# Kernel tuning notes

Hardware: AMD Instinct MI355X
Metric: run time of the kernel (lower is better)

## Reference

```python
import jax, jax.numpy as jnp
import numpy as np

HEADS = 6
EPS = 1e-5


def _na_idx(L, k, d):
    # NATTEN-style dilated neighborhood: work within dilation cosets,
    # clamp window to stay inside the image (window shifts at borders).
    i = np.arange(L)
    g = i % d
    p = i // d
    Lg = (L - g + d - 1) // d  # coset length per position
    start = np.clip(p - k // 2, 0, Lg - k)
    j = np.arange(k)
    nbr = g[:, None] + d * (start[:, None] + j[None, :])          # [L,k] neighbor coords
    rel = (start[:, None] + j[None, :]) - p[:, None] + (k - 1)    # [L,k] rpb index in [0,2k-2]
    return jnp.asarray(nbr, jnp.int32), jnp.asarray(rel, jnp.int32)


def _na2d(x, qkv_w, qkv_b, proj_w, proj_b, rpb, heads, k, d):
    # x: [B,H,W,C] NHWC neighborhood attention with relative positional bias
    B, H, W, C = x.shape
    dh = C // heads
    scale = dh ** -0.5
    qkv = (x @ qkv_w + qkv_b).reshape(B, H, W, 3, heads, dh)
    qkv = jnp.transpose(qkv, (3, 0, 4, 1, 2, 5))  # [3,B,h,H,W,dh]
    q, kk, v = qkv[0] * scale, qkv[1], qkv[2]
    nh, rh = _na_idx(H, k, d)
    nw, rw = _na_idx(W, k, d)

    def gather(t):  # [B,h,H,W,dh] -> [B,h,H,W,k,k,dh]
        t = t[:, :, nh]              # [B,h,H,k,W,dh]
        t = t[:, :, :, :, nw]        # [B,h,H,k,W,k,dh]
        return jnp.transpose(t, (0, 1, 2, 4, 3, 5, 6))

    kn, vn = gather(kk), gather(v)
    attn = jnp.einsum('bhxyd,bhxyijd->bhxyij', q, kn)  # [B,h,H,W,k,k]
    bias = rpb[:, rh]                  # [h,H,k,2k-1]
    bias = bias[:, :, :, rw]           # [h,H,k,W,k]
    bias = jnp.transpose(bias, (0, 1, 3, 2, 4))  # [h,H,W,k,k]
    attn = attn + bias[None]
    attn = jax.nn.softmax(attn.reshape(B, heads, H, W, k * k), axis=-1)
    attn = attn.reshape(B, heads, H, W, k, k)
    out = jnp.einsum('bhxyij,bhxyijd->bhxyd', attn, vn)
    out = jnp.transpose(out, (0, 2, 3, 1, 4)).reshape(B, H, W, C)
    return out @ proj_w + proj_b


def _rln(x, w, b, m1_w, m1_b, m2_w, m2_b):
    # Revised LayerNorm: normalize over (C,H,W) per sample; meta1/meta2 are 1x1 convs on std/mean
    mean = jnp.mean(x, axis=(1, 2, 3), keepdims=True)
    std = jnp.sqrt(jnp.mean((x - mean) ** 2, axis=(1, 2, 3), keepdims=True) + EPS)
    out = (x - mean) / std * w + b
    rescale = m1_w[None, :, None, None] * std + m1_b[None, :, None, None]
    rebias = m2_w[None, :, None, None] * mean + m2_b[None, :, None, None]
    return out, rescale, rebias


def _c11(x, w, b):  # 1x1 conv on NCHW == per-pixel linear
    return jnp.einsum('bchw,oc->bohw', x, w) + b[None, :, None, None]


def _gelu(x):
    return jax.nn.gelu(x, approximate=False)


def reference(x, ln_w, ln_b, m1_w, m1_b, m2_w, m2_b, qkv1_w, qkv1_b, proj1_w, proj1_b, rpb1, qkv2_w, qkv2_b, proj2_w, proj2_b, rpb2, mlp_w1, mlp_b1, mlp_w2, mlp_b2, bn_g, bn_b, bn_m, bn_v, pa_w1, pa_b1, pa_w2, pa_b2, ca_w1, ca_b1, ca_w2, ca_b2, m2a_w1, m2a_b1, m2a_w2, m2a_b2):
    # ---- NA block 1 (kernel 7, dilation 1) ----
    sc = x
    y, rs, rb = _rln(x, ln_w, ln_b, m1_w, m1_b, m2_w, m2_b)
    a = _na2d(jnp.transpose(y, (0, 2, 3, 1)), qkv1_w, qkv1_b, proj1_w, proj1_b, rpb1, HEADS, 7, 1)
    x = sc + jnp.transpose(a, (0, 3, 1, 2)) * rs + rb
    # ---- NA block 2 (kernel 5, dilation 8) ----
    sc = x
    y, rs, rb = _rln(x, ln_w, ln_b, m1_w, m1_b, m2_w, m2_b)
    a = _na2d(jnp.transpose(y, (0, 2, 3, 1)), qkv2_w, qkv2_b, proj2_w, proj2_b, rpb2, HEADS, 5, 8)
    x = sc + jnp.transpose(a, (0, 3, 1, 2)) * rs + rb
    # ---- MLP (source reuses the pre-attn2 shortcut `sc`) ----
    y, rs, rb = _rln(x, ln_w, ln_b, m1_w, m1_b, m2_w, m2_b)
    m = _c11(jax.nn.relu(_c11(y, mlp_w1, mlp_b1)), mlp_w2, mlp_b2)
    x = sc + m * rs + rb
    # ---- BN + pixel attention + channel attention + mlp2 ----
    sc = x
    inv = jax.lax.rsqrt(bn_v + EPS)
    y = (x - bn_m[None, :, None, None]) * (inv * bn_g)[None, :, None, None] + bn_b[None, :, None, None]
    pa = jax.nn.sigmoid(_c11(_gelu(_c11(y, pa_w1, pa_b1)), pa_w2, pa_b2))  # [B,1,H,W]
    y = pa * y
    gap = jnp.mean(y, axis=(2, 3), keepdims=True)
    ca = jax.nn.sigmoid(_c11(_gelu(_c11(gap, ca_w1, ca_b1)), ca_w2, ca_b2))  # [B,C,1,1]
    y = ca * y
    y = _c11(_gelu(_c11(y, m2a_w1, m2a_b1)), m2a_w2, m2a_b2)
    return sc + y


def setup_inputs() -> dict:
    key = jax.random.key(0)
    B, C, H, W, HID = 4, 96, 64, 64, 384
    ks = iter(jax.random.split(key, 48))

    def rn(shape, s=0.02):
        return jax.random.normal(next(ks), shape, jnp.float32) * s

    d = {}
    d['x'] = jax.random.normal(next(ks), (B, C, H, W), jnp.float32)
    d['ln_w'] = jnp.ones((1, C, 1, 1), jnp.float32)
    d['ln_b'] = jnp.zeros((1, C, 1, 1), jnp.float32)
    d['m1_w'] = rn((C,)); d['m1_b'] = jnp.ones((C,), jnp.float32)
    d['m2_w'] = rn((C,)); d['m2_b'] = jnp.zeros((C,), jnp.float32)
    d['qkv1_w'] = rn((C, 3 * C)); d['qkv1_b'] = jnp.zeros((3 * C,), jnp.float32)
    d['proj1_w'] = rn((C, C)); d['proj1_b'] = jnp.zeros((C,), jnp.float32)
    d['rpb1'] = rn((HEADS, 13, 13))
    d['qkv2_w'] = rn((C, 3 * C)); d['qkv2_b'] = jnp.zeros((3 * C,), jnp.float32)
    d['proj2_w'] = rn((C, C)); d['proj2_b'] = jnp.zeros((C,), jnp.float32)
    d['rpb2'] = rn((HEADS, 9, 9))
    d['mlp_w1'] = rn((HID, C)); d['mlp_b1'] = jnp.zeros((HID,), jnp.float32)
    d['mlp_w2'] = rn((C, HID)); d['mlp_b2'] = jnp.zeros((C,), jnp.float32)
    d['bn_g'] = jnp.ones((C,), jnp.float32); d['bn_b'] = jnp.zeros((C,), jnp.float32)
    d['bn_m'] = jnp.zeros((C,), jnp.float32); d['bn_v'] = jnp.ones((C,), jnp.float32)
    d['pa_w1'] = rn((C // 8, C)); d['pa_b1'] = jnp.zeros((C // 8,), jnp.float32)
    d['pa_w2'] = rn((1, C // 8)); d['pa_b2'] = jnp.zeros((1,), jnp.float32)
    d['ca_w1'] = rn((C, C)); d['ca_b1'] = jnp.zeros((C,), jnp.float32)
    d['ca_w2'] = rn((C, C)); d['ca_b2'] = jnp.zeros((C,), jnp.float32)
    d['m2a_w1'] = rn((C, C)); d['m2a_b1'] = jnp.zeros((C,), jnp.float32)
    d['m2a_w2'] = rn((C, C)); d['m2a_b2'] = jnp.zeros((C,), jnp.float32)
    return d
```

## Files before the change

kernel.cpp:

```cpp
#include <hip/hip_runtime.h>
#include <math.h>

#define CC 96
#define NP 4096
#define NHEADS 6
#define NELEMF 393216.0f
#define EPSF 1e-5f

typedef __attribute__((ext_vector_type(8))) short bf16x8;
typedef __attribute__((ext_vector_type(4))) float f32x4;
#define MFMA16(a,b,c) __builtin_amdgcn_mfma_f32_16x16x32_bf16(a,b,c,0,0,0)

#define WQKV1  64
#define WQKV2  (WQKV1+13824)
#define WPROJ1 (WQKV2+13824)
#define WPROJ2 (WPROJ1+4608)
#define WMLP1  (WPROJ2+4608)
#define WMLP2  (WMLP1+18432)
#define WM2A1  (WMLP2+18432)
#define WM2A2  (WM2A1+4608)
#define WPA1T  (WM2A2+4608)
#define WBNS   (WPA1T+1152)
#define WCA1T  (WBNS+192)
#define WCA2T  (WCA1T+9216)
#define WS_Q   870784
#define WS_K   (WS_Q+786432)
#define WS_V   (WS_K+786432)
#define WS_ATTPM (WS_V+786432)
#define WS_X1  (WS_ATTPM+786432)
#define WS_X2  (WS_X1+1572864)
#define WS_X3  (WS_X2+1572864)
#define WS_PA  (WS_X3+1572864)
#define WS_GAP (WS_PA+16384)

__device__ __forceinline__ float gelu_f(float x){
  return 0.5f * x * (1.0f + erff(x * 0.7071067811865476f));
}
__device__ __forceinline__ float sigmoid_f(float x){
  return 1.0f / (1.0f + __expf(-x));
}
__device__ __forceinline__ unsigned short bfr(float f){
  unsigned int u = __float_as_uint(f);
  u += 0x7fffu + ((u >> 16) & 1u);
  return (unsigned short)(u >> 16);
}
__device__ __forceinline__ float bflo16(unsigned short u){ return __uint_as_float(((unsigned int)u) << 16); }
__device__ __forceinline__ float bflo(unsigned int u){ return __uint_as_float(u << 16); }
__device__ __forceinline__ float bfhi(unsigned int u){ return __uint_as_float(u & 0xffff0000u); }
__device__ __forceinline__ void get_ms(const float* st, int b, float& mean, float& inv, float& stdv){
  float s = st[b], s2 = st[4+b];
  mean = s * (1.0f/NELEMF);
  float var = fmaxf(s2 * (1.0f/NELEMF) - mean*mean, 0.0f);
  stdv = sqrtf(var + EPSF);
  inv = 1.0f / stdv;
}
__device__ __forceinline__ float ldf(const float* p, int i){ return p[i]; }
__device__ __forceinline__ float ldf(const unsigned short* p, int i){ return bflo16(p[i]); }
__device__ __forceinline__ void load4(const float* p, float4& v){ v = *(const float4*)p; }
__device__ __forceinline__ void load4(const unsigned short* p, float4& v){
  ushort4 u = *(const ushort4*)p;
  v.x = bflo16(u.x); v.y = bflo16(u.y); v.z = bflo16(u.z); v.w = bflo16(u.w);
}

__global__ void prep_stats_kernel(const float* __restrict__ x, float* __restrict__ st,
                             const float* __restrict__ q1, const float* __restrict__ q2,
                             const float* __restrict__ p1, const float* __restrict__ p2,
                             const float* __restrict__ w1, const float* __restrict__ w2,
                             const float* __restrict__ a1, const float* __restrict__ a2,
                             const float* __restrict__ pw1,
                             const float* __restrict__ bg, const float* __restrict__ bb,
                             const float* __restrict__ bm, const float* __restrict__ bv,
                             const float* __restrict__ cw1, const float* __restrict__ cw2,
                             float* __restrict__ ws){
  if(blockIdx.x < 384){
    int b = blockIdx.x / CC, c = blockIdx.x % CC;
    const float4* p4 = (const float4*)(x + (size_t)(b*CC + c)*NP);
    float s = 0.f, s2 = 0.f;
    for(int i = threadIdx.x; i < 1024; i += 256){
      float4 v = p4[i];
      s += v.x + v.y + v.z + v.w;
      s2 = fmaf(v.x, v.x, fmaf(v.y, v.y, fmaf(v.z, v.z, fmaf(v.w, v.w, s2))));
    }
    for(int off = 32; off > 0; off >>= 1){ s += __shfl_down(s, off); s2 += __shfl_down(s2, off); }
    __shared__ float ls[8];
    int wid = threadIdx.x >> 6;
    if((threadIdx.x & 63) == 0){ ls[wid] = s; ls[4+wid] = s2; }
    __syncthreads();
    if(threadIdx.x == 0){
      atomicAdd(&st[b],   ls[0]+ls[1]+ls[2]+ls[3]);
      atomicAdd(&st[4+b], ls[4]+ls[5]+ls[6]+ls[7]);
    }
    return;
  }
  int gid = (blockIdx.x - 384)*256 + threadIdx.x;
  if(gid < 27648){ int n = gid/96, c = gid%96; ((unsigned short*)(ws+WQKV1))[gid] = bfr(q1[c*288+n]); }
  else if(gid < 55296){ int g = gid-27648; int n = g/96, c = g%96; ((unsigned short*)(ws+WQKV2))[g] = bfr(q2[c*288+n]); }
  else if(gid < 64512){ int g = gid-55296; int n = g/96, c = g%96; ((unsigned short*)(ws+WPROJ1))[g] = bfr(p1[c*96+n]); }
  else if(gid < 73728){ int g = gid-64512; int n = g/96, c = g%96; ((unsigned short*)(ws+WPROJ2))[g] = bfr(p2[c*96+n]); }
  else if(gid < 110592){ int g = gid-73728; ((unsigned short*)(ws+WMLP1))[g] = bfr(w1[g]); }
  else if(gid < 147456){ int g = gid-110592; ((unsigned short*)(ws+WMLP2))[g] = bfr(w2[g]); }
  else if(gid < 156672){ int g = gid-147456; ((unsigned short*)(ws+WM2A1))[g] = bfr(a1[g]); }
  else if(gid < 165888){ int g = gid-156672; ((unsigned short*)(ws+WM2A2))[g] = bfr(a2[g]); }
  else if(gid < 167040){ int g = gid-165888; int c = g/12, h = g%12; ws[WPA1T + g] = pw1[h*96+c]; }
  else if(gid < 167136){ int c = gid-167040;
    float sc = rsqrtf(bv[c] + EPSF) * bg[c];
    ws[WBNS + c] = sc;
    ws[WBNS + 96 + c] = bb[c] - bm[c]*sc;
  }
  else if(gid < 167520){ ws[WS_GAP + (gid-167136)] = 0.f; }
  else if(gid < 176736){ int g = gid-167520; int o = g/96, c = g%96; ws[WCA1T + c*96 + o] = cw1[g]; }
  else if(gid < 185952){ int g = gid-176736; int o = g/96, c = g%96; ws[WCA2T + c*96 + o] = cw2[g]; }
}

template<typename AT>
__global__ void __launch_bounds__(512) gemm_qkv_kernel(
    const AT* __restrict__ xin, const float* __restrict__ st,
    const float* __restrict__ lnw, const float* __restrict__ lnb,
    const unsigned short* __restrict__ wT, const float* __restrict__ qb,
    unsigned short* __restrict__ qo, unsigned short* __restrict__ ko, unsigned short* __restrict__ vo){
  __shared__ unsigned short Atl[64*104];
  __shared__ float scl[96], ofs[96];
  int m_base = blockIdx.x*64;
  int b = m_base >> 12, pxl0 = m_base & 4095;
  float mean, inv, stdv; get_ms(st, b, mean, inv, stdv);
  int tid = threadIdx.x;
  if(tid < 96){ float s = inv*lnw[tid]; scl[tid] = s; ofs[tid] = lnb[tid] - mean*s; }
  __syncthreads();
  const AT* src = xin + (size_t)b*CC*NP + pxl0;
  for(int idx = tid; idx < 96*16; idx += 512){
    int c = idx >> 4, p4 = (idx & 15) << 2;
    float4 v; load4(src + (size_t)c*NP + p4, v);
    float s = scl[c], o = ofs[c];
    Atl[(p4+0)*104 + c] = bfr(fmaf(v.x, s, o));
    Atl[(p4+1)*104 + c] = bfr(fmaf(v.y, s, o));
    Atl[(p4+2)*104 + c] = bfr(fmaf(v.z, s, o));
    Atl[(p4+3)*104 + c] = bfr(fmaf(v.w, s, o));
  }
  __syncthreads();
  int w = tid >> 6, lane = tid & 63, ml = lane & 15, q = lane >> 4;
  int row = w & 3, nh = w >> 2;
  const unsigned short* arow = Atl + (row*16 + ml)*104;
  bf16x8 av[3];
  #pragma unroll
  for(int ks = 0; ks < 3; ++ks) av[ks] = *(const bf16x8*)(arow + ks*32 + q*8);
  f32x4 z = {0.f,0.f,0.f,0.f};
  #pragma unroll
  for(int g0 = 0; g0 < 3; ++g0){
    int g = nh*3 + g0;
    f32x4 acc[3] = {z, z, z};
    #pragma unroll
    for(int ks = 0; ks < 3; ++ks){
      #pragma unroll
      for(int gg = 0; gg < 3; ++gg){
        bf16x8 bv = *(const bf16x8*)(wT + (g*48 + gg*16 + ml)*96 + ks*32 + q*8);
        acc[gg] = MFMA16(av[ks], bv, acc[gg]);
      }
    }
    #pragma unroll
    for(int gg = 0; gg < 3; ++gg){
      int nfb = g*48 + gg*16;
      int t = nfb/96, head = (nfb%96) >> 4;
      float scale = (t == 0) ? 0.25f : 1.0f;
      unsigned short* dst = (t == 0) ? qo : (t == 1) ? ko : vo;
      float bias = qb[nfb + ml];
      #pragma unroll
      for(int r = 0; r < 4; ++r){
        int pxl = pxl0 + row*16 + q*4 + r;
        dst[(((size_t)(b*NHEADS + head))*NP + pxl)*16 + ml] = bfr((acc[gg][r] + bias)*scale);
      }
    }
  }
}

template<typename SCT>
__global__ void __launch_bounds__(512) gemm_proj_kernel(
    const unsigned short* __restrict__ attpm, const unsigned short* __restrict__ wT,
    const float* __restrict__ pb, const SCT* __restrict__ scx, const float* __restrict__ st,
    const float* __restrict__ m1w, const float* __restrict__ m1b,
    const float* __restrict__ m2w, const float* __restrict__ m2b,
    unsigned short* __restrict__ dst, float* __restrict__ st_out){
  int w = threadIdx.x >> 6, lane = threadIdx.x & 63;
  int ml = lane & 15, q = lane >> 4;
  int m_base = blockIdx.x*128 + w*16;
  int n0 = blockIdx.y*48;
  f32x4 z = {0.f,0.f,0.f,0.f};
  f32x4 acc[3] = {z, z, z};
  {
    const bf16x8* a0 = (const bf16x8*)(attpm + (size_t)(m_base + ml)*96 + q*8);
    #pragma unroll
    for(int ks = 0; ks < 3; ++ks){
      bf16x8 av0 = a0[ks*4];
      #pragma unroll
      for(int g = 0; g < 3; ++g){
        bf16x8 bv = *(const bf16x8*)(wT + (n0 + g*16 + ml)*96 + ks*32 + q*8);
        acc[g] = MFMA16(av0, bv, acc[g]);
      }
    }
  }
  __shared__ float T[48*133];
  #pragma unroll
  for(int g = 0; g < 3; ++g)
    #pragma unroll
    for(int r = 0; r < 4; ++r)
      T[(g*16 + ml)*133 + w*16 + q*4 + r] = acc[g][r];
  __syncthreads();
  int b = (blockIdx.x*128) >> 12, pxl0 = (blockIdx.x*128) & 4095;
  float mean, inv, stdv; get_ms(st, b, mean, inv, stdv);
  float s = 0.f, s2 = 0.f;
  for(int idx = threadIdx.x; idx < 48*128; idx += 512){
    int row = idx >> 7, px = idx & 127;
    int n = n0 + row;
    float rsf = fmaf(m1w[n], stdv, m1b[n]);
    float rbf = fmaf(m2w[n], mean, m2b[n]);
    int ad = (b*CC + n)*NP + pxl0 + px;
    float val = ldf(scx, ad) + (T[row*133 + px] + pb[n])*rsf + rbf;
    dst[ad] = bfr(val);
    s += val; s2 = fmaf(val, val, s2);
  }
  for(int off = 32; off > 0; off >>= 1){ s += __shfl_down(s, off); s2 += __shfl_down(s2, off); }
  __shared__ float ls[16];
  int wid = threadIdx.x >> 6;
  if((threadIdx.x & 63) == 0){ ls[wid] = s; ls[8+wid] = s2; }
  __syncthreads();
  if(threadIdx.x == 0){
    atomicAdd(&st_out[b],   ls[0]+ls[1]+ls[2]+ls[3]+ls[4]+ls[5]+ls[6]+ls[7]);
    atomicAdd(&st_out[4+b], ls[8]+ls[9]+ls[10]+ls[11]+ls[12]+ls[13]+ls[14]+ls[15]);
  }
}

__global__ void __launch_bounds__(512) gemm_mlp_kernel(
    const unsigned short* __restrict__ xin, const float* __restrict__ st,
    const float* __restrict__ lnw, const float* __restrict__ lnb,
    const unsigned short* __restrict__ w1T, const float* __restrict__ b1,
    const unsigned short* __restrict__ w2T, const float* __restrict__ b2,
    const unsigned short* __restrict__ scx,
    const float* __restrict__ m1w, const float* __restrict__ m1b,
    const float* __restrict__ m2w, const float* __restrict__ m2b,
    float* __restrict__ dst){
  __shared__ __align__(16) char smbuf[63488];
  __shared__ float scl[96], ofs[96];
  unsigned short* Atl  = (unsigned short*)smbuf;
  unsigned short* hidL = (unsigned short*)(smbuf + 13312);
  float* T = (float*)(smbuf + 13312);
  int m_base = blockIdx.x*64;
  int b = m_base >> 12, pxl0 = m_base & 4095;
  float mean, inv, stdv; get_ms(st, b, mean, inv, stdv);
  int tid = threadIdx.x;
  if(tid < 96){ float s = inv*lnw[tid]; scl[tid] = s; ofs[tid] = lnb[tid] - mean*s; }
  __syncthreads();
  const unsigned short* src = xin + (size_t)b*CC*NP + pxl0;
  for(int idx = tid; idx < 96*16; idx += 512){
    int c = idx >> 4, p4 = (idx & 15) << 2;
    float4 v; load4(src + (size_t)c*NP + p4, v);
    float s = scl[c], o = ofs[c];
    Atl[(p4+0)*104 + c] = bfr(fmaf(v.x, s, o));
    Atl[(p4+1)*104 + c] = bfr(fmaf(v.y, s, o));
    Atl[(p4+2)*104 + c] = bfr(fmaf(v.z, s, o));
    Atl[(p4+3)*104 + c] = bfr(fmaf(v.w, s, o));
  }
  __syncthreads();
  int w = tid >> 6, lane = tid & 63, ml = lane & 15, q = lane >> 4;
  int row = w & 3, nh = w >> 2;
  f32x4 z = {0.f,0.f,0.f,0.f};
  {
    const unsigned short* arow = Atl + (row*16 + ml)*104;
    bf16x8 av[3];
    #pragma unroll
    for(int ks = 0; ks < 3; ++ks) av[ks] = *(const bf16x8*)(arow + ks*32 + q*8);
    #pragma unroll
    for(int g0 = 0; g0 < 4; ++g0){
      int g = nh*4 + g0;
      f32x4 acc[3] = {z, z, z};
      #pragma unroll
      for(int ks = 0; ks < 3; ++ks){
        #pragma unroll
        for(int gg = 0; gg < 3; ++gg){
          bf16x8 bv = *(const bf16x8*)(w1T + (g*48 + gg*16 + ml)*96 + ks*32 + q*8);
          acc[gg] = MFMA16(av[ks], bv, acc[gg]);
        }
      }
      #pragma unroll
      for(int gg = 0; gg < 3; ++gg){
        int n = g*48 + gg*16 + ml;
        float bias = b1[n];
        #pragma unroll
        for(int r = 0; r < 4; ++r)
          hidL[(row*16 + q*4 + r)*392 + n] = bfr(fmaxf(acc[gg][r] + bias, 0.f));
      }
    }
  }
  __syncthreads();
  f32x4 acc2[3] = {z, z, z};
  {
    const unsigned short* arow = hidL + (row*16 + ml)*392;
    #pragma unroll
    for(int ks = 0; ks < 12; ++ks){
      bf16x8 av = *(const bf16x8*)(arow + ks*32 + q*8);
      #pragma unroll
      for(int g0 = 0; g0 < 3; ++g0){
        int g = nh*3 + g0;
        bf16x8 bv = *(const bf16x8*)(w2T + (g*16 + ml)*384 + ks*32 + q*8);
        acc2[g0] = MFMA16(av, bv, acc2[g0]);
      }
    }
  }
  __syncthreads();
  #pragma unroll
  for(int g0 = 0; g0 < 3; ++g0){
    int g = nh*3 + g0;
    #pragma unroll
    for(int r = 0; r < 4; ++r)
      T[(g*16 + ml)*68 + row*16 + q*4 + r] = acc2[g0][r];
  }
  __syncthreads();
  for(int idx = tid; idx < 96*64; idx += 512){
    int n = idx >> 6, px = idx & 63;
    float rsf = fmaf(m1w[n], stdv, m1b[n]);
    float rbf = fmaf(m2w[n], mean, m2b[n]);
    int ad = (b*CC + n)*NP + pxl0 + px;
    dst[ad] = ldf(scx, ad) + (T[n*68 + px] + b2[n])*rsf + rbf;
  }
}

__global__ void __launch_bounds__(512) gemm_m2a_kernel(
    const float* __restrict__ x3, const float* __restrict__ bns,
    const float* __restrict__ pa, const float* __restrict__ gap,
    const float* __restrict__ cw1T, const float* __restrict__ cb1,
    const float* __restrict__ cw2T, const float* __restrict__ cb2,
    const unsigned short* __restrict__ w1T, const float* __restrict__ b1,
    const unsigned short* __restrict__ w2T, const float* __restrict__ b2,
    const float* __restrict__ scx, float* __restrict__ outp){
  __shared__ __align__(16) char smbuf[26624];
  __shared__ float scl[96], ofs[96], pal[64];
  __shared__ float gl[96], tl[96];
  unsigned short* Atl = (unsigned short*)smbuf;
  unsigned short* tl2 = (unsigned short*)(smbuf + 13312);
  float* T = (float*)smbuf;
  int m_base = blockIdx.x*64;
  int b = m_base >> 12, pxl0 = m_base & 4095;
  int tid = threadIdx.x;
  if(tid < 96) gl[tid] = gap[b*96 + tid];
  if(tid >= 128 && tid < 192) pal[tid-128] = pa[m_base + (tid-128)];
  __syncthreads();
  if(tid < 96){
    float a = cb1[tid];
    #pragma unroll 8
    for(int c = 0; c < 96; ++c) a = fmaf(gl[c], cw1T[c*96 + tid], a);
    tl[tid] = gelu_f(a);
  }
  __syncthreads();
  if(tid < 96){
    float a = cb2[tid];
    #pragma unroll 8
    for(int c = 0; c < 96; ++c) a = fmaf(tl[c], cw2T[c*96 + tid], a);
    float cv = sigmoid_f(a);
    scl[tid] = bns[tid]*cv; ofs[tid] = bns[96+tid]*cv;
  }
  __syncthreads();
  const float* src = x3 + (size_t)b*CC*NP + pxl0;
  for(int idx = tid; idx < 96*16; idx += 512){
    int c = idx >> 4, p4 = (idx & 15) << 2;
    float4 v = *(const float4*)(src + (size_t)c*NP + p4);
    float s = scl[c], o = ofs[c];
    Atl[(p4+0)*104 + c] = bfr(fmaf(v.x, s, o) * pal[p4+0]);
    Atl[(p4+1)*104 + c] = bfr(fmaf(v.y, s, o) * pal[p4+1]);
    Atl[(p4+2)*104 + c] = bfr(fmaf(v.z, s, o) * pal[p4+2]);
    Atl[(p4+3)*104 + c] = bfr(fmaf(v.w, s, o) * pal[p4+3]);
  }
  __syncthreads();
  int w = tid >> 6, lane = tid & 63, ml = lane & 15, q = lane >> 4;
  int row = w & 3, nh = w >> 2;
  f32x4 z = {0.f,0.f,0.f,0.f};
  f32x4 acc1[3] = {z, z, z};
  {
    const unsigned short* arow = Atl + (row*16 + ml)*104;
    #pragma unroll
    for(int ks = 0; ks < 3; ++ks){
      bf16x8 av = *(const bf16x8*)(arow + ks*32 + q*8);
      #pragma unroll
      for(int g0 = 0; g0 < 3; ++g0){
        int g = nh*3 + g0;
        bf16x8 bv = *(const bf16x8*)(w1T + (g*16 + ml)*96 + ks*32 + q*8);
        acc1[g0] = MFMA16(av, bv, acc1[g0]);
      }
    }
  }
  #pragma unroll
  for(int g0 = 0; g0 < 3; ++g0){
    int g = nh*3 + g0;
    float bias = b1[g*16 + ml];
    #pragma unroll
    for(int r = 0; r < 4; ++r)
      tl2[(row*16 + q*4 + r)*104 + g*16 + ml] = bfr(gelu_f(acc1[g0][r] + bias));
  }
  __syncthreads();
  f32x4 acc2[3] = {z, z, z};
  {
    const unsigned short* arow = tl2 + (row*16 + ml)*104;
    #pragma unroll
    for(int ks = 0; ks < 3; ++ks){
      bf16x8 av = *(const bf16x8*)(arow + ks*32 + q*8);
      #pragma unroll
      for(int g0 = 0; g0 < 3; ++g0){
        int g = nh*3 + g0;
        bf16x8 bv = *(const bf16x8*)(w2T + (g*16 + ml)*96 + ks*32 + q*8);
        acc2[g0] = MFMA16(av, bv, acc2[g0]);
      }
    }
  }
  __syncthreads();
  #pragma unroll
  for(int g0 = 0; g0 < 3; ++g0){
    int g = nh*3 + g0;
    #pragma unroll
    for(int r = 0; r < 4; ++r)
      T[(g*16 + ml)*68 + row*16 + q*4 + r] = acc2[g0][r];
  }
  __syncthreads();
  for(int idx = tid; idx < 96*64; idx += 512){
    int n = idx >> 6, p = idx & 63;
    int ad = (b*CC + n)*NP + pxl0 + p;
    outp[ad] = scx[ad] + T[n*68 + p] + b2[n];
  }
}

template<int K, int D, int RPB>
__global__ void __launch_bounds__(256) attn_kernel(
    const unsigned short* __restrict__ qb, const unsigned short* __restrict__ kb,
    const unsigned short* __restrict__ vb, const float* __restrict__ rpb,
    unsigned short* __restrict__ outp){
  int bh = blockIdx.x >> 6;
  int x = blockIdx.x & 63;
  int head = bh % NHEADS, b = bh / NHEADS;

  int gx = x % D, px = x / D;
  int Lgx = (64 - gx + D - 1) / D;
  int sx = min(max(px - K/2, 0), Lgx - K);

  __shared__ unsigned int sm[2*K*512];
  unsigned int* kl = sm;
  unsigned int* vl = sm + K*512;
  const unsigned int* kg = (const unsigned int*)(kb + (size_t)bh*NP*16);
  const unsigned int* vg = (const unsigned int*)(vb + (size_t)bh*NP*16);
  int tid = threadIdx.x;
  #pragma unroll
  for(int i = 0; i < K; ++i){
    int hh = gx + D*(sx + i);
    ((uint2*)(kl + i*512))[tid] = ((const uint2*)(kg + hh*512))[tid];
    ((uint2*)(vl + i*512))[tid] = ((const uint2*)(vg + hh*512))[tid];
  }
  __syncthreads();

  int pixoff = tid >> 2, t = tid & 3;
  int y = pixoff;
  int pix = x*64 + y;
  uint2 qd = *(const uint2*)(qb + ((size_t)bh*NP + pix)*16 + 4*t);
  float qx = bflo(qd.x), qy = bfhi(qd.x), qz = bflo(qd.y), qw = bfhi(qd.y);

  int gy = y % D, py = y / D;
  int Lgy = (64 - gy + D - 1) / D;
  int sy = min(max(py - K/2, 0), Lgy - K);

  float sc[K*K];
  #pragma unroll
  for(int i = 0; i < K; ++i){
    #pragma unroll
    for(int j = 0; j < K; ++j){
      int ww = gy + D*(sy + j);
      uint2 kv = *(const uint2*)(kl + i*512 + ww*8 + t*2);
      float s = qx*bflo(kv.x);
      s = fmaf(qy, bfhi(kv.x), s);
      s = fmaf(qz, bflo(kv.y), s);
      s = fmaf(qw, bfhi(kv.y), s);
      sc[i*K + j] = s;
    }
  }
  float mx = -1e30f;
  #pragma unroll
  for(int i = 0; i < K; ++i){
    const float* brow = rpb + (head*RPB + (sx + i - px + (K-1)))*RPB + (sy - py + (K-1));
    #pragma unroll
    for(int j = 0; j < K; ++j){
      float s = sc[i*K + j];
      s += __shfl_xor(s, 1);
      s += __shfl_xor(s, 2);
      s += brow[j];
      sc[i*K + j] = s;
      mx = fmaxf(mx, s);
    }
  }
  float sum = 0.f;
  #pragma unroll
  for(int n = 0; n < K*K; ++n){ float e = __expf(sc[n] - mx); sc[n] = e; sum += e; }
  float rs = 1.0f / sum;
  float4 acc = {0,0,0,0};
  #pragma unroll
  for(int i = 0; i < K; ++i){
    #pragma unroll
    for(int j = 0; j < K; ++j){
      int ww = gy + D*(sy + j);
      float wgt = sc[i*K + j] * rs;
      uint2 vv = *(const uint2*)(vl + i*512 + ww*8 + t*2);
      acc.x = fmaf(wgt, bflo(vv.x), acc.x);
      acc.y = fmaf(wgt, bfhi(vv.x), acc.y);
      acc.z = fmaf(wgt, bflo(vv.y), acc.z);
      acc.w = fmaf(wgt, bfhi(vv.y), acc.w);
    }
  }
  ushort4 o4;
  o4.x = bfr(acc.x); o4.y = bfr(acc.y); o4.z = bfr(acc.z); o4.w = bfr(acc.w);
  *(ushort4*)(outp + ((size_t)(b*NP + pix))*96 + head*16 + 4*t) = o4;
}

__global__ void __launch_bounds__(512) pa_gap_kernel(
    const float* __restrict__ x3, const float* __restrict__ bns,
    const float* __restrict__ w1t, const float* __restrict__ b1,
    const float* __restrict__ w2, const float* __restrict__ b2,
    float* __restrict__ pa, float* __restrict__ gap){
  int b = blockIdx.x >> 6;
  int px0 = (blockIdx.x & 63)*64;
  int pxq = threadIdx.x >> 3, t = threadIdx.x & 7;
  int p = px0 + pxq;
  float yvv[12];
  float acc[12];
  #pragma unroll
  for(int h = 0; h < 12; ++h) acc[h] = 0.f;
  #pragma unroll 6
  for(int cc = 0; cc < 12; ++cc){
    int c = t*12 + cc;
    float yv = fmaf(x3[(b*CC + c)*NP + p], bns[c], bns[96 + c]);
    yvv[cc] = yv;
    #pragma unroll
    for(int h = 0; h < 12; ++h) acc[h] = fmaf(yv, w1t[c*12 + h], acc[h]);
  }
  #pragma unroll
  for(int h = 0; h < 12; ++h){
    acc[h] += __shfl_xor(acc[h], 1);
    acc[h] += __shfl_xor(acc[h], 2);
    acc[h] += __shfl_xor(acc[h], 4);
  }
  float s = b2[0];
  #pragma unroll
  for(int h = 0; h < 12; ++h) s = fmaf(gelu_f(acc[h] + b1[h]), w2[h], s);
  float pav = sigmoid_f(s);
  if(t == 0) pa[b*NP + p] = pav;
  __shared__ float gpart[8*96];
  int w = threadIdx.x >> 6, lane = threadIdx.x & 63;
  #pragma unroll 6
  for(int cc = 0; cc < 12; ++cc){
    float g = yvv[cc] * pav;
    g += __shfl_xor(g, 8);  g += __shfl_xor(g, 16); g += __shfl_xor(g, 32);
    if(lane < 8) gpart[w*96 + lane*12 + cc] = g;
  }
  __syncthreads();
  if(threadIdx.x < 96){
    int c = threadIdx.x;
    float v = 0.f;
    #pragma unroll
    for(int ww = 0; ww < 8; ++ww) v += gpart[ww*96 + c];
    atomicAdd(&gap[b*96 + c], v * (1.0f/4096.0f));
  }
}

extern "C" void kernel_launch(void* const* d_in, const int* in_sizes, int n_in,
                              void* d_out, int out_size, void* d_ws, size_t ws_size,
                              hipStream_t stream){
  (void)in_sizes; (void)n_in; (void)out_size; (void)ws_size;
  const float* x     = (const float*)d_in[0];
  const float* lnw   = (const float*)d_in[1];
  const float* lnb   = (const float*)d_in[2];
  const float* m1w   = (const float*)d_in[3];
  const float* m1b   = (const float*)d_in[4];
  const float* m2w   = (const float*)d_in[5];
  const float* m2b   = (const float*)d_in[6];
  const float* qkv1w = (const float*)d_in[7];
  const float* qkv1b = (const float*)d_in[8];
  const float* proj1w= (const float*)d_in[9];
  const float* proj1b= (const float*)d_in[10];
  const float* rpb1  = (const float*)d_in[11];
  const float* qkv2w = (const float*)d_in[12];
  const float* qkv2b = (const float*)d_in[13];
  const float* proj2w= (const float*)d_in[14];
  const float* proj2b= (const float*)d_in[15];
  const float* rpb2  = (const float*)d_in[16];
  const float* mw1   = (const float*)d_in[17];
  const float* mb1   = (const float*)d_in[18];
  const float* mw2   = (const float*)d_in[19];
  const float* mb2   = (const float*)d_in[20];
  const float* bng   = (const float*)d_in[21];
  const float* bnb   = (const float*)d_in[22];
  const float* bnm   = (const float*)d_in[23];
  const float* bnv   = (const float*)d_in[24];
  const float* paw1  = (const float*)d_in[25];
  const float* pab1  = (const float*)d_in[26];
  const float* paw2  = (const float*)d_in[27];
  const float* pab2  = (const float*)d_in[28];
  const float* caw1  = (const float*)d_in[29];
  const float* cab1  = (const float*)d_in[30];
  const float* caw2  = (const float*)d_in[31];
  const float* cab2  = (const float*)d_in[32];
  const float* aw1   = (const float*)d_in[33];
  const float* ab1   = (const float*)d_in[34];
  const float* aw2   = (const float*)d_in[35];
  const float* ab2   = (const float*)d_in[36];

  float* ws  = (float*)d_ws;
  float* out = (float*)d_out;
  float* st0 = ws;
  float* st1 = ws + 8;
  float* st2 = ws + 16;
  unsigned short* q     = (unsigned short*)(ws + WS_Q);
  unsigned short* k     = (unsigned short*)(ws + WS_K);
  unsigned short* v     = (unsigned short*)(ws + WS_V);
  unsigned short* attpm = (unsigned short*)(ws + WS_ATTPM);
  unsigned short* x1b   = (unsigned short*)(ws + WS_X1);
  unsigned short* x2b   = (unsigned short*)(ws + WS_X2);
  float* x3  = ws + WS_X3;
  float* pab = ws + WS_PA;
  float* gpb = ws + WS_GAP;
  float* bns = ws + WBNS;

  hipMemsetAsync(d_ws, 0, 64*sizeof(float), stream);
  prep_stats_kernel<<<1111, 256, 0, stream>>>(x, st0, qkv1w, qkv2w, proj1w, proj2w,
                                              mw1, mw2, aw1, aw2, paw1,
                                              bng, bnb, bnm, bnv, caw1, caw2, ws);

  gemm_qkv_kernel<float><<<256, 512, 0, stream>>>(x, st0, lnw, lnb,
      (unsigned short*)(ws+WQKV1), qkv1b, q, k, v);
  attn_kernel<7,1,13><<<1536, 256, 0, stream>>>(q, k, v, rpb1, attpm);
  gemm_proj_kernel<float><<<dim3(128,2), 512, 0, stream>>>(attpm, (unsigned short*)(ws+WPROJ1),
      proj1b, x, st0, m1w, m1b, m2w, m2b, x1b, st1);

  gemm_qkv_kernel<unsigned short><<<256, 512, 0, stream>>>(x1b, st1, lnw, lnb,
      (unsigned short*)(ws+WQKV2), qkv2b, q, k, v);
  attn_kernel<5,8,9><<<1536, 256, 0, stream>>>(q, k, v, rpb2, attpm);
  gemm_proj_kernel<unsigned short><<<dim3(128,2), 512, 0, stream>>>(attpm, (unsigned short*)(ws+WPROJ2),
      proj2b, x1b, st1, m1w, m1b, m2w, m2b, x2b, st2);

  gemm_mlp_kernel<<<256, 512, 0, stream>>>(x2b, st2, lnw, lnb,
      (unsigned short*)(ws+WMLP1), mb1, (unsigned short*)(ws+WMLP2), mb2,
      x1b, m1w, m1b, m2w, m2b, x3);

  pa_gap_kernel<<<256, 512, 0, stream>>>(x3, bns, ws + WPA1T, pab1, paw2, pab2, pab, gpb);
  gemm_m2a_kernel<<<256, 512, 0, stream>>>(x3, bns, pab, gpb,
                                           ws + WCA1T, cab1, ws + WCA2T, cab2,
                                           (unsigned short*)(ws+WM2A1), ab1,
                                           (unsigned short*)(ws+WM2A2), ab2, x3, out);
}
```

Before: 274.3 us.

## Fuse neighborhood attention with output projection and residual LN stats

Merges the attention kernel and the projection GEMM into one kernel per attention stage. Each block handles one image row across all six heads, three heads at a time in separate LDS slots, and keeps the attention output in shared memory for the MFMA projection. This removes the global write and read of the intermediate attention tensor and two kernel launches. In exchange the grid shrinks to 256 large blocks with heavy LDS use, and the head pairs are processed serially, which reduces parallelism and latency hiding.

```diff
diff --git a/kernel.cpp b/kernel.cpp
--- a/kernel.cpp
+++ b/kernel.cpp
@@ -172,59 +172,149 @@
   }
 }
 
-template<typename SCT>
-__global__ void __launch_bounds__(512) gemm_proj_kernel(
-    const unsigned short* __restrict__ attpm, const unsigned short* __restrict__ wT,
-    const float* __restrict__ pb, const SCT* __restrict__ scx, const float* __restrict__ st,
+template<int K, int D, int RPB, typename SCT>
+__global__ void __launch_bounds__(768) attnproj_kernel(
+    const unsigned short* __restrict__ qb, const unsigned short* __restrict__ kb,
+    const unsigned short* __restrict__ vb, const float* __restrict__ rpb,
+    const unsigned short* __restrict__ wT, const float* __restrict__ pb,
+    const SCT* __restrict__ scx, const float* __restrict__ st,
     const float* __restrict__ m1w, const float* __restrict__ m1b,
     const float* __restrict__ m2w, const float* __restrict__ m2b,
     unsigned short* __restrict__ dst, float* __restrict__ st_out){
-  int w = threadIdx.x >> 6, lane = threadIdx.x & 63;
-  int ml = lane & 15, q = lane >> 4;
-  int m_base = blockIdx.x*128 + w*16;
-  int n0 = blockIdx.y*48;
+  __shared__ __align__(16) char smem[3*2*K*2048 + 13312];
+  __shared__ float ls[24];
+  unsigned int* kvb = (unsigned int*)smem;
+  unsigned short* attout = (unsigned short*)(smem + 3*2*K*2048);
+  float* T = (float*)smem;
+  int b = blockIdx.x >> 6;
+  int x = blockIdx.x & 63;
+  int tid = threadIdx.x;
+  int hseg = tid >> 8, tl = tid & 255;
+
+  int gx = x % D, px = x / D;
+  int Lgx = (64 - gx + D - 1) / D;
+  int sx = min(max(px - K/2, 0), Lgx - K);
+
+  unsigned int* kl = kvb + hseg*(2*K*512);
+  unsigned int* vl = kl + K*512;
+
+  int pixoff = tl >> 2, t = tl & 3;
+  int y = pixoff;
+  int pix = x*64 + y;
+  int gy = y % D, py = y / D;
+  int Lgy = (64 - gy + D - 1) / D;
+  int sy = min(max(py - K/2, 0), Lgy - K);
+
+  for(int hp = 0; hp < 2; ++hp){
+    int head = hp*3 + hseg;
+    int bh = b*NHEADS + head;
+    const unsigned int* kg = (const unsigned int*)(kb + (size_t)bh*NP*16);
+    const unsigned int* vg = (const unsigned int*)(vb + (size_t)bh*NP*16);
+    #pragma unroll
+    for(int i = 0; i < K; ++i){
+      int hh = gx + D*(sx + i);
+      ((uint2*)(kl + i*512))[tl] = ((const uint2*)(kg + hh*512))[tl];
+      ((uint2*)(vl + i*512))[tl] = ((const uint2*)(vg + hh*512))[tl];
+    }
+    uint2 qd = *(const uint2*)(qb + ((size_t)bh*NP + pix)*16 + 4*t);
+    float qx = bflo(qd.x), qy = bfhi(qd.x), qz = bflo(qd.y), qw = bfhi(qd.y);
+    __syncthreads();
+
+    float sc[K*K];
+    #pragma unroll
+    for(int i = 0; i < K; ++i){
+      #pragma unroll
+      for(int j = 0; j < K; ++j){
+        int ww = gy + D*(sy + j);
+        uint2 kv2 = *(const uint2*)(kl + i*512 + ww*8 + t*2);
+        float s = qx*bflo(kv2.x);
+        s = fmaf(qy, bfhi(kv2.x), s);
+        s = fmaf(qz, bflo(kv2.y), s);
+        s = fmaf(qw, bfhi(kv2.y), s);
+        sc[i*K + j] = s;
+      }
+    }
+    float mx = -1e30f;
+    #pragma unroll
+    for(int i = 0; i < K; ++i){
+      const float* brow = rpb + (head*RPB + (sx + i - px + (K-1)))*RPB + (sy - py + (K-1));
+      #pragma unroll
+      for(int j = 0; j < K; ++j){
+        float s = sc[i*K + j];
+        s += __shfl_xor(s, 1);
+        s += __shfl_xor(s, 2);
+        s += brow[j];
+        sc[i*K + j] = s;
+        mx = fmaxf(mx, s);
+      }
+    }
+    float sum = 0.f;
+    #pragma unroll
+    for(int n = 0; n < K*K; ++n){ float e = __expf(sc[n] - mx); sc[n] = e; sum += e; }
+    float rs = 1.0f / sum;
+    float4 acc = {0,0,0,0};
+    #pragma unroll
+    for(int i = 0; i < K; ++i){
+      #pragma unroll
+      for(int j = 0; j < K; ++j){
+        int ww = gy + D*(sy + j);
+        float wgt = sc[i*K + j] * rs;
+        uint2 vv = *(const uint2*)(vl + i*512 + ww*8 + t*2);
+        acc.x = fmaf(wgt, bflo(vv.x), acc.x);
+        acc.y = fmaf(wgt, bfhi(vv.x), acc.y);
+        acc.z = fmaf(wgt, bflo(vv.y), acc.z);
+        acc.w = fmaf(wgt, bfhi(vv.y), acc.w);
+      }
+    }
+    ushort4 o4;
+    o4.x = bfr(acc.x); o4.y = bfr(acc.y); o4.z = bfr(acc.z); o4.w = bfr(acc.w);
+    *(ushort4*)(attout + pixoff*104 + head*16 + 4*t) = o4;
+    __syncthreads();
+  }
+
+  int w = tid >> 6, lane = tid & 63, ml = lane & 15, q = lane >> 4;
+  int rg = w & 3, nh = w >> 2;
   f32x4 z = {0.f,0.f,0.f,0.f};
-  f32x4 acc[3] = {z, z, z};
+  f32x4 acc[2] = {z, z};
   {
-    const bf16x8* a0 = (const bf16x8*)(attpm + (size_t)(m_base + ml)*96 + q*8);
+    const unsigned short* arow = attout + (rg*16 + ml)*104;
     #pragma unroll
     for(int ks = 0; ks < 3; ++ks){
-      bf16x8 av0 = a0[ks*4];
-      #pragma unroll
-      for(int g = 0; g < 3; ++g){
-        bf16x8 bv = *(const bf16x8*)(wT + (n0 + g*16 + ml)*96 + ks*32 + q*8);
-        acc[g] = MFMA16(av0, bv, acc[g]);
-      }
-    }
-  }
-  __shared__ float T[48*133];
-  #pragma unroll
-  for(int g = 0; g < 3; ++g)
+      bf16x8 av = *(const bf16x8*)(arow + ks*32 + q*8);
+      #pragma unroll
+      for(int g = 0; g < 2; ++g){
+        bf16x8 bv = *(const bf16x8*)(wT + (nh*32 + g*16 + ml)*96 + ks*32 + q*8);
+        acc[g] = MFMA16(av, bv, acc[g]);
+      }
+    }
+  }
+  #pragma unroll
+  for(int g = 0; g < 2; ++g)
     #pragma unroll
     for(int r = 0; r < 4; ++r)
-      T[(g*16 + ml)*133 + w*16 + q*4 + r] = acc[g][r];
-  __syncthreads();
-  int b = (blockIdx.x*128) >> 12, pxl0 = (blockIdx.x*128) & 4095;
+      T[(nh*32 + g*16 + ml)*68 + rg*16 + q*4 + r] = acc[g][r];
+  __syncthreads();
+  int pxl0 = x*64;
   float mean, inv, stdv; get_ms(st, b, mean, inv, stdv);
   float s = 0.f, s2 = 0.f;
-  for(int idx = threadIdx.x; idx < 48*128; idx += 512){
-    int row = idx >> 7, px = idx & 127;
-    int n = n0 + row;
+  for(int idx = tid; idx < 96*64; idx += 768){
+    int n = idx >> 6, p = idx & 63;
     float rsf = fmaf(m1w[n], stdv, m1b[n]);
     float rbf = fmaf(m2w[n], mean, m2b[n]);
-    int ad = (b*CC + n)*NP + pxl0 + px;
-    float val = ldf(scx, ad) + (T[row*133 + px] + pb[n])*rsf + rbf;
+    int ad = (b*CC + n)*NP + pxl0 + p;
+    float val = ldf(scx, ad) + (T[n*68 + p] + pb[n])*rsf + rbf;
     dst[ad] = bfr(val);
     s += val; s2 = fmaf(val, val, s2);
   }
   for(int off = 32; off > 0; off >>= 1){ s += __shfl_down(s, off); s2 += __shfl_down(s2, off); }
-  __shared__ float ls[16];
-  int wid = threadIdx.x >> 6;
-  if((threadIdx.x & 63) == 0){ ls[wid] = s; ls[8+wid] = s2; }
-  __syncthreads();
-  if(threadIdx.x == 0){
-    atomicAdd(&st_out[b],   ls[0]+ls[1]+ls[2]+ls[3]+ls[4]+ls[5]+ls[6]+ls[7]);
-    atomicAdd(&st_out[4+b], ls[8]+ls[9]+ls[10]+ls[11]+ls[12]+ls[13]+ls[14]+ls[15]);
+  if(lane == 0){ ls[w] = s; ls[12+w] = s2; }
+  __syncthreads();
+  if(tid == 0){
+    float a0 = 0.f, a1 = 0.f;
+    #pragma unroll
+    for(int i = 0; i < 12; ++i){ a0 += ls[i]; a1 += ls[12+i]; }
+    atomicAdd(&st_out[b], a0);
+    atomicAdd(&st_out[4+b], a1);
   }
 }
 
@@ -422,94 +512,6 @@
     int ad = (b*CC + n)*NP + pxl0 + p;
     outp[ad] = scx[ad] + T[n*68 + p] + b2[n];
   }
-}
-
-template<int K, int D, int RPB>
-__global__ void __launch_bounds__(256) attn_kernel(
-    const unsigned short* __restrict__ qb, const unsigned short* __restrict__ kb,
-    const unsigned short* __restrict__ vb, const float* __restrict__ rpb,
-    unsigned short* __restrict__ outp){
-  int bh = blockIdx.x >> 6;
-  int x = blockIdx.x & 63;
-  int head = bh % NHEADS, b = bh / NHEADS;
-
-  int gx = x % D, px = x / D;
-  int Lgx = (64 - gx + D - 1) / D;
-  int sx = min(max(px - K/2, 0), Lgx - K);
-
-  __shared__ unsigned int sm[2*K*512];
-  unsigned int* kl = sm;
-  unsigned int* vl = sm + K*512;
-  const unsigned int* kg = (const unsigned int*)(kb + (size_t)bh*NP*16);
-  const unsigned int* vg = (const unsigned int*)(vb + (size_t)bh*NP*16);
-  int tid = threadIdx.x;
-  #pragma unroll
-  for(int i = 0; i < K; ++i){
-    int hh = gx + D*(sx + i);
-    ((uint2*)(kl + i*512))[tid] = ((const uint2*)(kg + hh*512))[tid];
-    ((uint2*)(vl + i*512))[tid] = ((const uint2*)(vg + hh*512))[tid];
-  }
-  __syncthreads();
-
-  int pixoff = tid >> 2, t = tid & 3;
-  int y = pixoff;
-  int pix = x*64 + y;
-  uint2 qd = *(const uint2*)(qb + ((size_t)bh*NP + pix)*16 + 4*t);
-  float qx = bflo(qd.x), qy = bfhi(qd.x), qz = bflo(qd.y), qw = bfhi(qd.y);
-
-  int gy = y % D, py = y / D;
-  int Lgy = (64 - gy + D - 1) / D;
-  int sy = min(max(py - K/2, 0), Lgy - K);
-
-  float sc[K*K];
-  #pragma unroll
-  for(int i = 0; i < K; ++i){
-    #pragma unroll
-    for(int j = 0; j < K; ++j){
-      int ww = gy + D*(sy + j);
-      uint2 kv = *(const uint2*)(kl + i*512 + ww*8 + t*2);
-      float s = qx*bflo(kv.x);
-      s = fmaf(qy, bfhi(kv.x), s);
-      s = fmaf(qz, bflo(kv.y), s);
-      s = fmaf(qw, bfhi(kv.y), s);
-      sc[i*K + j] = s;
-    }
-  }
-  float mx = -1e30f;
-  #pragma unroll
-  for(int i = 0; i < K; ++i){
-    const float* brow = rpb + (head*RPB + (sx + i - px + (K-1)))*RPB + (sy - py + (K-1));
-    #pragma unroll
-    for(int j = 0; j < K; ++j){
-      float s = sc[i*K + j];
-      s += __shfl_xor(s, 1);
-      s += __shfl_xor(s, 2);
-      s += brow[j];
-      sc[i*K + j] = s;
-      mx = fmaxf(mx, s);
-    }
-  }
-  float sum = 0.f;
-  #pragma unroll
-  for(int n = 0; n < K*K; ++n){ float e = __expf(sc[n] - mx); sc[n] = e; sum += e; }
-  float rs = 1.0f / sum;
-  float4 acc = {0,0,0,0};
-  #pragma unroll
-  for(int i = 0; i < K; ++i){
-    #pragma unroll
-    for(int j = 0; j < K; ++j){
-      int ww = gy + D*(sy + j);
-      float wgt = sc[i*K + j] * rs;
-      uint2 vv = *(const uint2*)(vl + i*512 + ww*8 + t*2);
-      acc.x = fmaf(wgt, bflo(vv.x), acc.x);
-      acc.y = fmaf(wgt, bfhi(vv.x), acc.y);
-      acc.z = fmaf(wgt, bflo(vv.y), acc.z);
-      acc.w = fmaf(wgt, bfhi(vv.y), acc.w);
-    }
-  }
-  ushort4 o4;
-  o4.x = bfr(acc.x); o4.y = bfr(acc.y); o4.z = bfr(acc.z); o4.w = bfr(acc.w);
-  *(ushort4*)(outp + ((size_t)(b*NP + pix))*96 + head*16 + 4*t) = o4;
 }
 
 __global__ void __launch_bounds__(512) pa_gap_kernel(
@@ -612,7 +614,6 @@
   unsigned short* q     = (unsigned short*)(ws + WS_Q);
   unsigned short* k     = (unsigned short*)(ws + WS_K);
   unsigned short* v     = (unsigned short*)(ws + WS_V);
-  unsigned short* attpm = (unsigned short*)(ws + WS_ATTPM);
   unsigned short* x1b   = (unsigned short*)(ws + WS_X1);
   unsigned short* x2b   = (unsigned short*)(ws + WS_X2);
   float* x3  = ws + WS_X3;
@@ -627,15 +628,13 @@
 
   gemm_qkv_kernel<float><<<256, 512, 0, stream>>>(x, st0, lnw, lnb,
       (unsigned short*)(ws+WQKV1), qkv1b, q, k, v);
-  attn_kernel<7,1,13><<<1536, 256, 0, stream>>>(q, k, v, rpb1, attpm);
-  gemm_proj_kernel<float><<<dim3(128,2), 512, 0, stream>>>(attpm, (unsigned short*)(ws+WPROJ1),
-      proj1b, x, st0, m1w, m1b, m2w, m2b, x1b, st1);
+  attnproj_kernel<7,1,13,float><<<256, 768, 0, stream>>>(q, k, v, rpb1,
+      (unsigned short*)(ws+WPROJ1), proj1b, x, st0, m1w, m1b, m2w, m2b, x1b, st1);
 
   gemm_qkv_kernel<unsigned short><<<256, 512, 0, stream>>>(x1b, st1, lnw, lnb,
       (unsigned short*)(ws+WQKV2), qkv2b, q, k, v);
-  attn_kernel<5,8,9><<<1536, 256, 0, stream>>>(q, k, v, rpb2, attpm);
-  gemm_proj_kernel<unsigned short><<<dim3(128,2), 512, 0, stream>>>(attpm, (unsigned short*)(ws+WPROJ2),
-      proj2b, x1b, st1, m1w, m1b, m2w, m2b, x2b, st2);
+  attnproj_kernel<5,8,9,unsigned short><<<256, 768, 0, stream>>>(q, k, v, rpb2,
+      (unsigned short*)(ws+WPROJ2), proj2b, x1b, st1, m1w, m1b, m2w, m2b, x2b, st2);
 
   gemm_mlp_kernel<<<256, 512, 0, stream>>>(x2b, st2, lnw, lnb,
       (unsigned short*)(ws+WMLP1), mb1, (unsigned short*)(ws+WMLP2), mb2,
```

Measured after the change: 355.4 us. 1.3x slower.
